# Kernel optimization log

Measured on AMD Instinct MI355X. Metric: run time of the kernel, lower is better.

The kernel has to match this reference:

```python
import jax, jax.numpy as jnp
import numpy as np
from jax import lax

L, C, H, W = 3, 64, 32, 32   # layer_num, new_size channels/spatial
N = H * W                    # 1024 attention positions
B = 8


def _conv(x, w, b, stride, pad):
    out = lax.conv_general_dilated(
        x, w, (stride, stride), [(pad, pad), (pad, pad)],
        dimension_numbers=('NCHW', 'OIHW', 'NCHW'))
    return out + b[None, :, None, None]


def setup_inputs() -> dict:
    key = jax.random.key(0)
    ks = iter(jax.random.split(key, 40))
    def rn(shape, scale=1.0):
        return (jax.random.normal(next(ks), shape) * scale).astype(jnp.float32)
    inp = {
        'src0': rn((B, 128, 64, 64)), 'src1': rn((B, 256, 32, 32)), 'src2': rn((B, 512, 32, 32)),
        'tgt0': rn((B, 128, 64, 64)), 'tgt1': rn((B, 256, 32, 32)), 'tgt2': rn((B, 512, 32, 32)),
    }
    # Project/Fit convs: layer0 is stride-2 3x3 (64->32), layers 1,2 are 1x1
    for pre, ic, k in [('fs0', 128, 3), ('fs1', 256, 1), ('fs2', 512, 1),
                       ('ft0', 128, 3), ('ft1', 256, 1), ('ft2', 512, 1)]:
        inp[pre + '_w'] = rn((C, ic, k, k), (ic * k * k) ** -0.5)
        inp[pre + '_b'] = rn((C,), 0.01)
    # PAM query/key/value and CAM value 1x1 convs, stacked over layers
    for pre in ['pq', 'pk', 'pv', 'cv']:
        inp[pre + '_w'] = rn((L, C, C), C ** -0.5)
        inp[pre + '_b'] = rn((L, C), 0.01)
    return inp


def reference(src0, src1, src2, tgt0, tgt1, tgt2,
              fs0_w, fs0_b, fs1_w, fs1_b, fs2_w, fs2_b,
              ft0_w, ft0_b, ft1_w, ft1_b, ft2_w, ft2_b,
              pq_w, pq_b, pk_w, pk_b, pv_w, pv_b, cv_w, cv_b):
    # Project: Fit each source/target to [B,C,H,W]
    S = jnp.stack([_conv(src0, fs0_w, fs0_b, 2, 1),
                   _conv(src1, fs1_w, fs1_b, 1, 0),
                   _conv(src2, fs2_w, fs2_b, 1, 0)])   # [L,B,C,H,W]
    T = jnp.stack([_conv(tgt0, ft0_w, ft0_b, 2, 1),
                   _conv(tgt1, ft1_w, ft1_b, 1, 0),
                   _conv(tgt2, ft2_w, ft2_b, 1, 0)])
    S = S.reshape(L, B, C, N)
    T = T.reshape(L, B, C, N)

    # ---- PAM: position attention over all (target i, source j) pairs ----
    q = jnp.einsum('ioc,ibcn->ibon', pq_w, T) + pq_b[:, None, :, None]
    k = jnp.einsum('joc,jbcn->jbon', pk_w, S) + pk_b[:, None, :, None]
    v = jnp.einsum('ioc,ibcn->ibon', pv_w, T) + pv_b[:, None, :, None]
    e_pam = jnp.einsum('ibcn,jbcm->ijbnm', q, k)          # [L,L,B,N,N]
    alpha_pam = jax.nn.softmax(lax.stop_gradient(e_pam.mean(axis=(2, 3, 4))), axis=-1)
    attn_pam = jax.nn.softmax(e_pam, axis=-1).sum(axis=1)  # sum over sources j -> [L,B,N,N]
    # out[b,c,n] = sum_m v[b,c,m] * attn[b,n,m]  (value @ attention^T)
    out_pam = jnp.einsum('ibcm,ibnm->ibcn', v, attn_pam)

    # ---- CAM: channel attention over all pairs ----
    e_cam = jnp.einsum('ibcn,jbdn->ijbcd', T, S)           # [L,L,B,C,C]
    alpha_cam = jax.nn.softmax(lax.stop_gradient(e_cam.mean(axis=(2, 3, 4))), axis=-1)
    attn_cam = jax.nn.softmax(e_cam, axis=-1).sum(axis=1)  # [L,B,C,C]
    vc = jnp.einsum('ioc,ibcn->ibon', cv_w, T) + cv_b[:, None, :, None]
    out_cam = jnp.einsum('ibcd,ibdn->ibcn', attn_cam, vc)

    fused = ((out_pam + out_cam) * 0.5).reshape(L, B, C * N)
    alpha = (alpha_cam + alpha_pam) * 0.5                  # [L,L]
    srcs = S.reshape(L, B, C * N)
    # DAAttention appends fused_i then projected target_i per layer (order preserved)
    tgts = jnp.stack([fused, T.reshape(L, B, C * N)], axis=1).reshape(2 * L, B, C * N)
    return (srcs, alpha, tgts)
```

## Files before the change

kernel.cpp:

```cpp
#include <hip/hip_runtime.h>

static constexpr int L_ = 3, B_ = 8, C_ = 64, N_ = 1024;
static constexpr int PLANE = C_ * N_;
static constexpr int SZ    = L_ * B_ * PLANE;
static constexpr int BPL   = B_ * PLANE;

#define DI __device__ __forceinline__

typedef _Float16 h8 __attribute__((ext_vector_type(8)));
typedef __attribute__((ext_vector_type(4))) float f32x4;
typedef unsigned int uint32;

DI float wred_sum(float v) {
#pragma unroll
  for (int m = 1; m < 64; m <<= 1) v += __shfl_xor(v, m, 64);
  return v;
}

DI unsigned short f2h(float f) {
  return __builtin_bit_cast(unsigned short, (_Float16)f);
}
DI float h2f(unsigned short h) {
  return (float)__builtin_bit_cast(_Float16, h);
}
DI uint32 pkh(float a, float b) {
  return (uint32)f2h(a) | ((uint32)f2h(b) << 16);
}
DI h8 bch8(uint4 v) { return __builtin_bit_cast(h8, v); }

DI f32x4 mfmah(h8 a, h8 b, f32x4 c) {
  return __builtin_amdgcn_mfma_f32_16x16x32_f16(a, b, c, 0, 0, 0);
}

DI void xprep_body(const float* __restrict__ ing, unsigned short* __restrict__ og,
                   int K, int N, int t, float tl[64][65])
{
#pragma unroll 4
  for (int r = 0; r < 16; ++r) {
    const int kk = r * 4 + (t >> 6);
    tl[kk][t & 63] = ing[(size_t)kk * N + (t & 63)];
  }
  __syncthreads();
  const int mm = t >> 2, kseg = (t & 3) * 16;
  uint32 hw[8];
#pragma unroll
  for (int ii = 0; ii < 8; ++ii)
    hw[ii] = pkh(tl[kseg + 2 * ii][mm], tl[kseg + 2 * ii + 1][mm]);
  unsigned short* o = og + (size_t)mm * K + kseg;
  uint4 h0; h0.x = hw[0]; h0.y = hw[1]; h0.z = hw[2]; h0.w = hw[3];
  uint4 h1; h1.x = hw[4]; h1.y = hw[5]; h1.z = hw[6]; h1.w = hw[7];
  *reinterpret_cast<uint4*>(o)     = h0;
  *reinterpret_cast<uint4*>(o + 8) = h1;
}

__global__ __launch_bounds__(256) void xprep_conv_kernel(
    const float* __restrict__ in_s, const float* __restrict__ in_t,
    unsigned short* __restrict__ o_s, unsigned short* __restrict__ o_t)
{
  __shared__ float tl[64][65];
  const int g = blockIdx.x & 7, ts = blockIdx.x >> 3;
  const int kc = blockIdx.y, nc = blockIdx.z;
  const float* in = ts ? in_t : in_s;
  unsigned short* out = ts ? o_t : o_s;
  const float* ing = in + (size_t)g * 128 * 4096 + (size_t)(kc * 64) * 4096 + nc * 64;
  unsigned short* og = out + ((size_t)g * 4096 + nc * 64) * 128 + kc * 64;
  xprep_body(ing, og, 128, 4096, threadIdx.x, tl);
}

__global__ __launch_bounds__(256) void xprep_fit_kernel(
    const float* __restrict__ s1, const float* __restrict__ s2,
    const float* __restrict__ t1, const float* __restrict__ t2,
    unsigned short* __restrict__ x1, unsigned short* __restrict__ x2,
    unsigned short* __restrict__ x3, unsigned short* __restrict__ x4)
{
  __shared__ float tl[64][65];
  const int g = blockIdx.x & 7, ts = blockIdx.x >> 3;
  const int K = (ts & 1) ? 512 : 256;
  const int kc = blockIdx.y, nc = blockIdx.z;
  if (kc >= (K >> 6)) return;
  const float* in = (ts == 0) ? s1 : (ts == 1) ? s2 : (ts == 2) ? t1 : t2;
  unsigned short* out = (ts == 0) ? x1 : (ts == 1) ? x2 : (ts == 2) ? x3 : x4;
  const float* ing = in + (size_t)g * K * 1024 + (size_t)(kc * 64) * 1024 + nc * 64;
  unsigned short* og = out + ((size_t)g * 1024 + nc * 64) * K + kc * 64;
  xprep_body(ing, og, K, 1024, threadIdx.x, tl);
}

__global__ __launch_bounds__(256) void w9conv_kernel(
    const float* __restrict__ w_s, const float* __restrict__ w_t,
    unsigned short* __restrict__ w9_s, unsigned short* __restrict__ w9_t)
{
  const int e = blockIdx.x * 256 + threadIdx.x;
  const float* w = (e < 73728) ? w_s : w_t;
  unsigned short* o = (e < 73728) ? w9_s : w9_t;
  const int le = (e < 73728) ? e : e - 73728;
  const int ci = le & 127;
  const int q = le >> 7;
  const int co = q & 63;
  const int k9 = q >> 6;
  o[le] = f2h(w[(co * 128 + ci) * 9 + k9]);
}

__global__ __launch_bounds__(256) void conv0_mfma_kernel(
    const unsigned short* __restrict__ inT_s, const unsigned short* __restrict__ inT_t,
    const unsigned short* __restrict__ w9_s, const unsigned short* __restrict__ w9_t,
    const float* __restrict__ b_s, const float* __restrict__ b_t,
    float* __restrict__ Sout, float* __restrict__ Tout, float* __restrict__ tdup)
{
  const int yr = blockIdx.x;
  const int b  = blockIdx.y;
  const int st = blockIdx.z;
  const unsigned short* inT = st ? inT_t : inT_s;
  const unsigned short* w9  = st ? w9_t  : w9_s;
  const float* bias = st ? b_t : b_s;
  float* outA = st ? Tout : Sout;

  const int t = threadIdx.x, lane = t & 63;
  const int ct = t >> 6;
  const int nl = lane & 15, g16 = lane >> 4;
  const unsigned short* inb = inT + (size_t)b * (4096 * 128);
  const unsigned short* wbase = w9 + (size_t)(ct * 16 + nl) * 128;

  f32x4 acc0 = f32x4{0.f, 0.f, 0.f, 0.f};
  f32x4 acc1 = f32x4{0.f, 0.f, 0.f, 0.f};
  const uint4 zz = uint4{0u, 0u, 0u, 0u};

#pragma unroll 1
  for (int tap = 0; tap < 9; ++tap) {
    const int ky = tap / 3, kx = tap - 3 * (tap / 3);
    const int py = 2 * yr - 1 + ky;
    const int px0 = 2 * nl - 1 + kx;
    const int px1 = px0 + 32;
    const bool v0 = (py >= 0) && (px0 >= 0);
    const bool v1 = (py >= 0);
    const unsigned short* prow = inb + (ptrdiff_t)py * (64 * 128);
#pragma unroll
    for (int ks = 0; ks < 4; ++ks) {
      const h8 a = bch8(*reinterpret_cast<const uint4*>(
          wbase + tap * 8192 + ks * 32 + g16 * 8));
      const uint4 bv0 = v0 ? *reinterpret_cast<const uint4*>(
                                 prow + px0 * 128 + ks * 32 + g16 * 8) : zz;
      const uint4 bv1 = v1 ? *reinterpret_cast<const uint4*>(
                                 prow + px1 * 128 + ks * 32 + g16 * 8) : zz;
      acc0 = mfmah(a, bch8(bv0), acc0);
      acc1 = mfmah(a, bch8(bv1), acc1);
    }
  }

  const int yb = yr * 32;
#pragma unroll
  for (int r = 0; r < 4; ++r) {
    const int co = ct * 16 + g16 * 4 + r;
    const float bv = bias[co];
    const int idx = (b * 64 + co) * 1024 + yb + nl;
    const float o0 = acc0[r] + bv;
    const float o1 = acc1[r] + bv;
    outA[idx] = o0; outA[idx + 16] = o1;
    if (st) { tdup[idx] = o0; tdup[idx + 16] = o1; }
  }
}

__global__ __launch_bounds__(256) void gemm64_kernel(
    const float* __restrict__ W, int wstride, int wdiv,
    const float* __restrict__ X, int xstride,
    float* __restrict__ out, int ostride,
    const float* __restrict__ bias, int bstride,
    int K)
{
  const int g  = blockIdx.x;
  const int n0 = blockIdx.y * 64;
  const float* Wg = W + (size_t)(g / wdiv) * wstride;
  const float* Xg = X + (size_t)g * xstride;
  const int t = threadIdx.x;
  __shared__ float Xs[32][64];
  __shared__ float Ws[32][64];
  const int tn = t & 15, cgp = t >> 4;
  const int n4 = tn * 4, co4 = cgp * 4;
  float acc[4][4] = {};

  for (int k0 = 0; k0 < K; k0 += 32) {
    {
      const int kk = t >> 4;
      const int nn = (t & 15) * 4;
      *reinterpret_cast<float4*>(&Xs[kk][nn]) =
          *reinterpret_cast<const float4*>(Xg + (size_t)(k0 + kk) * N_ + n0 + nn);
      *reinterpret_cast<float4*>(&Xs[kk + 16][nn]) =
          *reinterpret_cast<const float4*>(Xg + (size_t)(k0 + kk + 16) * N_ + n0 + nn);
    }
    {
      const int co = t & 63, q4 = t >> 6;
      const float* wp = Wg + (size_t)co * K + k0 + q4 * 8;
      const float4 a = *reinterpret_cast<const float4*>(wp);
      const float4 c = *reinterpret_cast<const float4*>(wp + 4);
      const int kb = q4 * 8;
      Ws[kb + 0][co] = a.x; Ws[kb + 1][co] = a.y; Ws[kb + 2][co] = a.z; Ws[kb + 3][co] = a.w;
      Ws[kb + 4][co] = c.x; Ws[kb + 5][co] = c.y; Ws[kb + 6][co] = c.z; Ws[kb + 7][co] = c.w;
    }
    __syncthreads();
#pragma unroll
    for (int kk = 0; kk < 32; ++kk) {
      const float4 xv = *reinterpret_cast<const float4*>(&Xs[kk][n4]);
      const float4 wv = *reinterpret_cast<const float4*>(&Ws[kk][co4]);
      const float xa[4] = {xv.x, xv.y, xv.z, xv.w};
      const float wa[4] = {wv.x, wv.y, wv.z, wv.w};
#pragma unroll
      for (int a = 0; a < 4; ++a)
#pragma unroll
        for (int b2 = 0; b2 < 4; ++b2)
          acc[a][b2] = fmaf(wa[a], xa[b2], acc[a][b2]);
    }
    __syncthreads();
  }

  float bv[4] = {0.f, 0.f, 0.f, 0.f};
  if (bias) {
    const float* bg = bias + (size_t)(g / wdiv) * bstride;
    bv[0] = bg[co4]; bv[1] = bg[co4 + 1]; bv[2] = bg[co4 + 2]; bv[3] = bg[co4 + 3];
  }
#pragma unroll
  for (int ii = 0; ii < 4; ++ii) {
    float4 o4;
    o4.x = acc[ii][0] + bv[ii]; o4.y = acc[ii][1] + bv[ii];
    o4.z = acc[ii][2] + bv[ii]; o4.w = acc[ii][3] + bv[ii];
    *reinterpret_cast<float4*>(out + (size_t)g * ostride + (co4 + ii) * N_ + n0 + n4) = o4;
  }
}

__global__ __launch_bounds__(256) void proj_kernel(
    const float* __restrict__ Tm, const float* __restrict__ Sm,
    const float* __restrict__ wq, const float* __restrict__ wk,
    const float* __restrict__ wv2, const float* __restrict__ wc,
    const float* __restrict__ bq, const float* __restrict__ bk,
    const float* __restrict__ bv2, const float* __restrict__ bc,
    unsigned short* __restrict__ qT, unsigned short* __restrict__ kT,
    unsigned short* __restrict__ vh, float* __restrict__ vcb)
{
  const int g  = blockIdx.x;
  const int n0 = blockIdx.y * 64;
  const int z  = blockIdx.z;
  const float* W  = (z == 0) ? wq : (z == 1) ? wk : (z == 2) ? wv2 : wc;
  const float* bi = (z == 0) ? bq : (z == 1) ? bk : (z == 2) ? bv2 : bc;
  const float* Xg = ((z == 1) ? Sm : Tm) + (size_t)g * PLANE;
  const float* Wg = W + (g >> 3) * 4096;
  const float* bg = bi + (g >> 3) * 64;

  const int t = threadIdx.x;
  __shared__ float Xs[32][64];
  __shared__ float Ws[32][64];
  const int tn = t & 15, cgp = t >> 4;
  const int n4 = tn * 4, co4 = cgp * 4;
  float acc[4][4] = {};

#pragma unroll 1
  for (int k0 = 0; k0 < 64; k0 += 32) {
    {
      const int kk = t >> 4;
      const int nn = (t & 15) * 4;
      *reinterpret_cast<float4*>(&Xs[kk][nn]) =
          *reinterpret_cast<const float4*>(Xg + (size_t)(k0 + kk) * N_ + n0 + nn);
      *reinterpret_cast<float4*>(&Xs[kk + 16][nn]) =
          *reinterpret_cast<const float4*>(Xg + (size_t)(k0 + kk + 16) * N_ + n0 + nn);
    }
    {
      const int co = t & 63, q4 = t >> 6;
      const float* wp = Wg + (size_t)co * 64 + k0 + q4 * 8;
      const float4 a = *reinterpret_cast<const float4*>(wp);
      const float4 c = *reinterpret_cast<const float4*>(wp + 4);
      const int kb = q4 * 8;
      Ws[kb + 0][co] = a.x; Ws[kb + 1][co] = a.y; Ws[kb + 2][co] = a.z; Ws[kb + 3][co] = a.w;
      Ws[kb + 4][co] = c.x; Ws[kb + 5][co] = c.y; Ws[kb + 6][co] = c.z; Ws[kb + 7][co] = c.w;
    }
    __syncthreads();
#pragma unroll
    for (int kk = 0; kk < 32; ++kk) {
      const float4 xv = *reinterpret_cast<const float4*>(&Xs[kk][n4]);
      const float4 wv = *reinterpret_cast<const float4*>(&Ws[kk][co4]);
      const float xa[4] = {xv.x, xv.y, xv.z, xv.w};
      const float wa[4] = {wv.x, wv.y, wv.z, wv.w};
#pragma unroll
      for (int a = 0; a < 4; ++a)
#pragma unroll
        for (int b2 = 0; b2 < 4; ++b2)
          acc[a][b2] = fmaf(wa[a], xa[b2], acc[a][b2]);
    }
    __syncthreads();
  }

  float bvv[4];
#pragma unroll
  for (int ii = 0; ii < 4; ++ii) bvv[ii] = bg[co4 + ii];

  if (z <= 1) {
    unsigned short* out = (z == 0 ? qT : kT);
#pragma unroll
    for (int jj = 0; jj < 4; ++jj) {
      const size_t base = ((size_t)g * 1024 + n0 + n4 + jj) * 64 + co4;
      uint2 w2;
      w2.x = pkh(acc[0][jj] + bvv[0], acc[1][jj] + bvv[1]);
      w2.y = pkh(acc[2][jj] + bvv[2], acc[3][jj] + bvv[3]);
      *reinterpret_cast<uint2*>(out + base) = w2;
    }
  } else if (z == 2) {
#pragma unroll
    for (int ii = 0; ii < 4; ++ii) {
      const size_t base = ((size_t)g * 64 + co4 + ii) * 1024 + n0 + n4;
      uint2 w2;
      w2.x = pkh(acc[ii][0] + bvv[ii], acc[ii][1] + bvv[ii]);
      w2.y = pkh(acc[ii][2] + bvv[ii], acc[ii][3] + bvv[ii]);
      *reinterpret_cast<uint2*>(vh + base) = w2;
    }
  } else {
    float* out = vcb + (size_t)g * PLANE;
#pragma unroll
    for (int ii = 0; ii < 4; ++ii) {
      float4 o4;
      o4.x = acc[ii][0] + bvv[ii]; o4.y = acc[ii][1] + bvv[ii];
      o4.z = acc[ii][2] + bvv[ii]; o4.w = acc[ii][3] + bvv[ii];
      *reinterpret_cast<float4*>(out + (co4 + ii) * N_ + n0 + n4) = o4;
    }
  }
}

__global__ __launch_bounds__(256) void whconv_kernel(
    const float* __restrict__ w1s, const float* __restrict__ w2s,
    const float* __restrict__ w1t, const float* __restrict__ w2t,
    unsigned short* __restrict__ wh)
{
  const int p = blockIdx.x * 256 + threadIdx.x;
  const float* in; int local; unsigned short* out;
  if (p < 8192)       { in = w1s; local = p;         out = wh; }
  else if (p < 24576) { in = w2s; local = p - 8192;  out = wh + 16384; }
  else if (p < 32768) { in = w1t; local = p - 24576; out = wh + 49152; }
  else                { in = w2t; local = p - 32768; out = wh + 65536; }
  const float2 v = *reinterpret_cast<const float2*>(in + 2 * local);
  *reinterpret_cast<uint32*>(out + 2 * local) = pkh(v.x, v.y);
}

__global__ __launch_bounds__(256) void gemmh_kernel(
    const unsigned short* __restrict__ Xa, const unsigned short* __restrict__ Xb,
    const unsigned short* __restrict__ Wa, const unsigned short* __restrict__ Wb,
    const float* __restrict__ ba, const float* __restrict__ bb,
    float* __restrict__ oa, float* __restrict__ ob, float* __restrict__ o2b,
    int K)
{
  const int g = blockIdx.x;
  const bool isb = g >= 8;
  const int gl = g & 7;
  const unsigned short* X = (isb ? Xb : Xa) + (size_t)gl * 1024 * K;
  const unsigned short* W = isb ? Wb : Wa;
  const float* bias = isb ? bb : ba;
  float* out = (isb ? ob : oa) + (size_t)gl * PLANE;
  float* out2 = isb ? o2b + (size_t)gl * PLANE : nullptr;

  const int t = threadIdx.x, lane = t & 63, wv = t >> 6;
  const int nl = lane & 15, g16 = lane >> 4;
  const int n0w = blockIdx.y * 64 + wv * 16;

  const unsigned short* xp = X + (size_t)(n0w + nl) * K + g16 * 8;
  const unsigned short* wp = W + (size_t)nl * K + g16 * 8;

  f32x4 acc[4];
#pragma unroll
  for (int ct = 0; ct < 4; ++ct) acc[ct] = f32x4{0.f, 0.f, 0.f, 0.f};

#pragma unroll 4
  for (int kk = 0; kk < K; kk += 32) {
    const h8 a = bch8(*reinterpret_cast<const uint4*>(xp + kk));
#pragma unroll
    for (int ct = 0; ct < 4; ++ct) {
      const h8 bfr = bch8(*reinterpret_cast<const uint4*>(wp + (size_t)ct * 16 * K + kk));
      acc[ct] = mfmah(a, bfr, acc[ct]);
    }
  }

#pragma unroll
  for (int ct = 0; ct < 4; ++ct) {
    const int co = ct * 16 + nl;
    const float bv = bias[co];
    float4 o4;
    o4.x = acc[ct][0] + bv; o4.y = acc[ct][1] + bv;
    o4.z = acc[ct][2] + bv; o4.w = acc[ct][3] + bv;
    const int idx = co * N_ + n0w + g16 * 4;
    *reinterpret_cast<float4*>(out + idx) = o4;
    if (out2) {
      out2[idx] = o4.x; out2[idx + 1] = o4.y;
      out2[idx + 2] = o4.z; out2[idx + 3] = o4.w;
    }
  }
}

__global__ __launch_bounds__(256) void ecam_kernel(
    const float* __restrict__ T, const float* __restrict__ S,
    float* __restrict__ ecam, float* __restrict__ esum_cam)
{
  const int bx = blockIdx.x;
  const int b = bx & 7;
  const int j = (bx >> 3) % 3;
  const int i = bx / 24;
  const int ych = blockIdx.y;
  const float* Tg = T + (size_t)(i * 8 + b) * PLANE;
  const float* Sg = S + (size_t)(j * 8 + b) * PLANE;
  const int t = threadIdx.x;
  __shared__ float Ts[64 * 68];
  __shared__ float Ss[64 * 68];
  __shared__ float rs[4];
  float acc[4][4] = {};
  const int c0 = (t & 15) * 4, d0 = (t >> 4) * 4;

  for (int nb = ych * 256; nb < ych * 256 + 256; nb += 64) {
    __syncthreads();
    {
      const int nn = t & 63, rb = t >> 6;
#pragma unroll
      for (int r = 0; r < 16; ++r) {
        const int row = rb * 16 + r;
        Ts[nn * 68 + row] = Tg[row * N_ + nb + nn];
        Ss[nn * 68 + row] = Sg[row * N_ + nb + nn];
      }
    }
    __syncthreads();
#pragma unroll 8
    for (int nn = 0; nn < 64; ++nn) {
      const float4 tv = *reinterpret_cast<const float4*>(&Ts[nn * 68 + c0]);
      const float4 sv = *reinterpret_cast<const float4*>(&Ss[nn * 68 + d0]);
      const float ta[4] = {tv.x, tv.y, tv.z, tv.w};
      const float sa[4] = {sv.x, sv.y, sv.z, sv.w};
#pragma unroll
      for (int ci = 0; ci < 4; ++ci)
#pragma unroll
        for (int di = 0; di < 4; ++di)
          acc[ci][di] = fmaf(ta[ci], sa[di], acc[ci][di]);
    }
  }
  float s = 0.f;
#pragma unroll
  for (int ci = 0; ci < 4; ++ci)
#pragma unroll
    for (int di = 0; di < 4; ++di) s += acc[ci][di];
  s = wred_sum(s);
  if ((t & 63) == 0) rs[t >> 6] = s;
  __syncthreads();
  if (t == 0) atomicAdd(esum_cam + i * 3 + j, rs[0] + rs[1] + rs[2] + rs[3]);

  float* eo = ecam + (size_t)((i * 3 + j) * 8 + b) * 4096;
#pragma unroll
  for (int ci = 0; ci < 4; ++ci)
#pragma unroll
    for (int di = 0; di < 4; ++di)
      atomicAdd(eo + (c0 + ci) * 64 + d0 + di, acc[ci][di]);
}

__global__ __launch_bounds__(256) void acam_kernel(
    const float* __restrict__ ecam, float* __restrict__ acam)
{
  const int bx = blockIdx.x;
  const int b = bx & 7, i = bx >> 3;
  const int t = threadIdx.x;
  const int c = t >> 2, seg = t & 3;
  float acc[16] = {};
#pragma unroll
  for (int j = 0; j < 3; ++j) {
    const float* e = ecam + (size_t)((i * 3 + j) * 8 + b) * 4096 + c * 64 + seg * 16;
    float ev[16];
#pragma unroll
    for (int r = 0; r < 4; ++r) {
      const float4 v4 = *reinterpret_cast<const float4*>(e + r * 4);
      ev[4 * r] = v4.x; ev[4 * r + 1] = v4.y; ev[4 * r + 2] = v4.z; ev[4 * r + 3] = v4.w;
    }
    float mx = ev[0];
#pragma unroll
    for (int r = 1; r < 16; ++r) mx = fmaxf(mx, ev[r]);
    mx = fmaxf(mx, __shfl_xor(mx, 1, 4));
    mx = fmaxf(mx, __shfl_xor(mx, 2, 4));
    float pv[16], ss = 0.f;
#pragma unroll
    for (int r = 0; r < 16; ++r) { pv[r] = __expf(ev[r] - mx); ss += pv[r]; }
    ss += __shfl_xor(ss, 1, 4);
    ss += __shfl_xor(ss, 2, 4);
    const float rc = 1.f / ss;
#pragma unroll
    for (int r = 0; r < 16; ++r) acc[r] += pv[r] * rc;
  }
  float* ao = acam + (size_t)(i * 8 + b) * 4096 + c * 64 + seg * 16;
#pragma unroll
  for (int r = 0; r < 4; ++r) {
    float4 o4; o4.x = acc[4 * r]; o4.y = acc[4 * r + 1]; o4.z = acc[4 * r + 2]; o4.w = acc[4 * r + 3];
    *reinterpret_cast<float4*>(ao + r * 4) = o4;
  }
}

__global__ __launch_bounds__(512, 4) void pam_mfma_kernel(
    const unsigned short* __restrict__ qT, const unsigned short* __restrict__ kT,
    const unsigned short* __restrict__ vh,
    const float* __restrict__ ocam, float* __restrict__ tgts, float* __restrict__ esum_pam)
{
  const int bx = blockIdx.x;
  const int qt = bx & 63;
  const int b  = (bx >> 6) & 7;
  const int i  = bx >> 9;
  const int n0 = qt * 16;
  const int t = threadIdx.x;
  const int lane = t & 63;
  const int wv = t >> 6;
  const int nl = lane & 15;
  const int g16 = lane >> 4;

  __shared__ unsigned short Plds[16 * 1024];
  __shared__ float osum[64 * 16];
  __shared__ float redmx[128];
  __shared__ float redse[128];
  __shared__ float redes[8];

  const size_t ibo = (size_t)(i * 8 + b) * PLANE;
  const size_t gbase = (size_t)(i * 8 + b) * 1024;

  const unsigned short* qp = qT + (gbase + n0 + nl) * 64 + g16 * 8;
  const h8 qh0 = bch8(*reinterpret_cast<const uint4*>(qp));
  const h8 qh1 = bch8(*reinterpret_cast<const uint4*>(qp + 32));

  const int wm0 = wv * 128;
  const int ct = wv & 3;
  const int mh = wv >> 2;

#pragma unroll 1
  for (int j = 0; j < 3; ++j) {
    const unsigned short* kp =
        kT + ((size_t)(j * 8 + b) * 1024 + wm0 + nl) * 64 + g16 * 8;

    f32x4 l4[8];
#pragma unroll
    for (int hh = 0; hh < 2; ++hh) {
      uint4 kf[8];
#pragma unroll
      for (int tt = 0; tt < 4; ++tt) {
        const int off = (hh * 4 + tt) * 1024;
        kf[2 * tt]     = *reinterpret_cast<const uint4*>(kp + off);
        kf[2 * tt + 1] = *reinterpret_cast<const uint4*>(kp + off + 32);
      }
#pragma unroll
      for (int tt = 0; tt < 4; ++tt) {
        f32x4 a = f32x4{0.f, 0.f, 0.f, 0.f};
        a = mfmah(bch8(kf[2 * tt]), qh0, a);
        a = mfmah(bch8(kf[2 * tt + 1]), qh1, a);
        l4[hh * 4 + tt] = a;
      }
    }

    float pm = -3.4e38f, es = 0.f;
#pragma unroll
    for (int tt = 0; tt < 8; ++tt) {
#pragma unroll
      for (int r = 0; r < 4; ++r) { pm = fmaxf(pm, l4[tt][r]); es += l4[tt][r]; }
    }
    pm = fmaxf(pm, __shfl_xor(pm, 16, 64));
    pm = fmaxf(pm, __shfl_xor(pm, 32, 64));
    es = wred_sum(es);
    if (lane < 16) redmx[wv * 16 + lane] = pm;
    if (lane == 0) redes[wv] = es;
    __syncthreads();
    float mx = redmx[nl];
#pragma unroll
    for (int w = 1; w < 8; ++w) mx = fmaxf(mx, redmx[w * 16 + nl]);
    if (t == 0) {
      float s = 0.f;
#pragma unroll
      for (int w = 0; w < 8; ++w) s += redes[w];
      atomicAdd(esum_pam + i * 3 + j, s);
    }

    float ps = 0.f;
#pragma unroll
    for (int tt = 0; tt < 8; ++tt) {
#pragma unroll
      for (int r = 0; r < 4; ++r) {
        l4[tt][r] = __expf(l4[tt][r] - mx);
        ps += l4[tt][r];
      }
    }
    ps += __shfl_xor(ps, 16, 64);
    ps += __shfl_xor(ps, 32, 64);
    if (lane < 16) redse[wv * 16 + lane] = ps;
    __syncthreads();
    float den = redse[nl];
#pragma unroll
    for (int w = 1; w < 8; ++w) den += redse[w * 16 + nl];
    const float rs = 1.f / den;

#pragma unroll
    for (int tt = 0; tt < 8; ++tt) {
      const int m = wm0 + tt * 16 + g16 * 4;
      unsigned short* pp = &Plds[nl * 1024 + (m ^ (nl * 8))];
      float p0 = l4[tt][0] * rs, p1 = l4[tt][1] * rs;
      float p2 = l4[tt][2] * rs, p3 = l4[tt][3] * rs;
      if (j > 0) {
        const uint2 old = *reinterpret_cast<const uint2*>(pp);
        p0 += h2f((unsigned short)(old.x & 0xffffu));
        p1 += h2f((unsigned short)(old.x >> 16));
        p2 += h2f((unsigned short)(old.y & 0xffffu));
        p3 += h2f((unsigned short)(old.y >> 16));
      }
      uint2 w2; w2.x = pkh(p0, p1); w2.y = pkh(p2, p3);
      *reinterpret_cast<uint2*>(pp) = w2;
    }
  }

  __syncthreads();

  const unsigned short* vg = vh + ibo + (size_t)(ct * 16 + nl) * 1024 + mh * 512 + g16 * 8;
  f32x4 oa = f32x4{0.f, 0.f, 0.f, 0.f};
#pragma unroll
  for (int hh = 0; hh < 2; ++hh) {
    uint4 vf[8];
#pragma unroll
    for (int u = 0; u < 8; ++u)
      vf[u] = *reinterpret_cast<const uint4*>(vg + (hh * 8 + u) * 32);
#pragma unroll
    for (int u = 0; u < 8; ++u) {
      const int ml = mh * 512 + (hh * 8 + u) * 32 + g16 * 8;
      const uint4 pf = *reinterpret_cast<const uint4*>(&Plds[nl * 1024 + (ml ^ (nl * 8))]);
      oa = mfmah(bch8(vf[u]), bch8(pf), oa);
    }
  }

  if (mh == 0) {
#pragma unroll
    for (int r = 0; r < 4; ++r)
      osum[(ct * 16 + g16 * 4 + r) * 16 + nl] = oa[r];
  }
  __syncthreads();
  if (mh == 1) {
    const float* og = ocam + ibo;
    float* outg = tgts + (size_t)(2 * i * 8 + b) * PLANE;
#pragma unroll
    for (int r = 0; r < 4; ++r) {
      const int c = ct * 16 + g16 * 4 + r;
      const int idx = c * N_ + n0 + nl;
      outg[idx] = 0.5f * (oa[r] + osum[c * 16 + nl] + og[idx]);
    }
  }
}

__global__ void alpha_kernel(const float* __restrict__ esum, float* __restrict__ alpha)
{
  const int t = threadIdx.x;
  if (t >= 9) return;
  const int i = t / 3, j = t % 3;
  float p[3], c[3];
#pragma unroll
  for (int jj = 0; jj < 3; ++jj) {
    p[jj] = esum[i * 3 + jj] * (1.0f / 8388608.0f);
    c[jj] = esum[9 + i * 3 + jj] * (1.0f / 32768.0f);
  }
  const float mp = fmaxf(p[0], fmaxf(p[1], p[2]));
  const float mc = fmaxf(c[0], fmaxf(c[1], c[2]));
  float sp = 0.f, sc = 0.f;
#pragma unroll
  for (int jj = 0; jj < 3; ++jj) { sp += __expf(p[jj] - mp); sc += __expf(c[jj] - mc); }
  alpha[t] = 0.5f * (__expf(p[j] - mp) / sp + __expf(c[j] - mc) / sc);
}

extern "C" void kernel_launch(void* const* d_in, const int* in_sizes, int n_in,
                              void* d_out, int out_size, void* d_ws, size_t ws_size,
                              hipStream_t stream)
{
  const float* src0 = (const float*)d_in[0];
  const float* src1 = (const float*)d_in[1];
  const float* src2 = (const float*)d_in[2];
  const float* tgt0 = (const float*)d_in[3];
  const float* tgt1 = (const float*)d_in[4];
  const float* tgt2 = (const float*)d_in[5];
  const float* fs0_w = (const float*)d_in[6];  const float* fs0_b = (const float*)d_in[7];
  const float* fs1_w = (const float*)d_in[8];  const float* fs1_b = (const float*)d_in[9];
  const float* fs2_w = (const float*)d_in[10]; const float* fs2_b = (const float*)d_in[11];
  const float* ft0_w = (const float*)d_in[12]; const float* ft0_b = (const float*)d_in[13];
  const float* ft1_w = (const float*)d_in[14]; const float* ft1_b = (const float*)d_in[15];
  const float* ft2_w = (const float*)d_in[16]; const float* ft2_b = (const float*)d_in[17];
  const float* pq_w = (const float*)d_in[18];  const float* pq_b = (const float*)d_in[19];
  const float* pk_w = (const float*)d_in[20];  const float* pk_b = (const float*)d_in[21];
  const float* pv_w = (const float*)d_in[22];  const float* pv_b = (const float*)d_in[23];
  const float* cv_w = (const float*)d_in[24];  const float* cv_b = (const float*)d_in[25];

  float* out = (float*)d_out;
  float* S     = out;
  float* alpha = out + SZ;
  float* tgts  = out + SZ + 9;

  float* ws   = (float*)d_ws;
  float* T    = ws;
  float* qb   = ws + (size_t)SZ;
  float* kb   = ws + (size_t)2 * SZ;
  float* vcb  = ws + (size_t)4 * SZ;
  float* ocam = ws + (size_t)5 * SZ;
  float* ecam = ws + (size_t)6 * SZ;
  float* acam = ws + (size_t)6 * SZ + 294912;
  float* esum = ws + (size_t)6 * SZ + 393216;

  unsigned short* kT = (unsigned short*)(ws + (size_t)6 * SZ + 393216 + 256);
  unsigned short* vh = kT + (size_t)24 * PLANE;
  unsigned short* wh = vh + (size_t)24 * PLANE;
  unsigned short* w9s = wh + 98304;
  unsigned short* w9t = w9s + 73728;
  unsigned short* qT = (unsigned short*)kb;

  unsigned short* inTs = (unsigned short*)qb;
  unsigned short* inTt = inTs + 4194304;
  unsigned short* Xs1 = (unsigned short*)qb;
  unsigned short* Xs2 = Xs1 + 2097152;
  unsigned short* Xt1 = Xs1 + 6291456;
  unsigned short* Xt2 = Xs1 + 8388608;

  hipMemsetAsync(esum, 0, 18 * sizeof(float), stream);
  hipMemsetAsync(ecam, 0, 294912 * sizeof(float), stream);

  w9conv_kernel<<<576, 256, 0, stream>>>(fs0_w, ft0_w, w9s, w9t);
  xprep_conv_kernel<<<dim3(16, 2, 64), 256, 0, stream>>>(src0, tgt0, inTs, inTt);
  conv0_mfma_kernel<<<dim3(32, 8, 2), 256, 0, stream>>>(
      inTs, inTt, w9s, w9t, fs0_b, ft0_b, S, T, tgts + (size_t)1 * BPL);

  xprep_fit_kernel<<<dim3(32, 8, 16), 256, 0, stream>>>(
      src1, src2, tgt1, tgt2, Xs1, Xs2, Xt1, Xt2);
  whconv_kernel<<<192, 256, 0, stream>>>(fs1_w, fs2_w, ft1_w, ft2_w, wh);
  gemmh_kernel<<<dim3(16, 16), 256, 0, stream>>>(
      Xs1, Xt1, wh, wh + 49152, fs1_b, ft1_b,
      S + BPL, T + BPL, tgts + (size_t)3 * BPL, 256);
  gemmh_kernel<<<dim3(16, 16), 256, 0, stream>>>(
      Xs2, Xt2, wh + 16384, wh + 65536, fs2_b, ft2_b,
      S + 2 * BPL, T + 2 * BPL, tgts + (size_t)5 * BPL, 512);

  proj_kernel<<<dim3(24, 16, 4), 256, 0, stream>>>(
      T, S, pq_w, pk_w, pv_w, cv_w, pq_b, pk_b, pv_b, cv_b, qT, kT, vh, vcb);

  ecam_kernel<<<dim3(72, 4), 256, 0, stream>>>(T, S, ecam, esum + 9);
  acam_kernel<<<24, 256, 0, stream>>>(ecam, acam);
  gemm64_kernel<<<dim3(24, 16), 256, 0, stream>>>(acam, 4096, 1, vcb, PLANE, ocam, PLANE,
                                                  nullptr, 0, 64);

  pam_mfma_kernel<<<1536, 512, 0, stream>>>(qT, kT, vh, ocam, tgts, esum);

  alpha_kernel<<<1, 64, 0, stream>>>(esum, alpha);
}
```

Baseline: 296.8 us.

## Merge weight-prep and 1x1 GEMM launches; single-barrier online softmax in PAM

The two weight-conversion kernels become one launch, and the two gemmh launches for the K=256 and K=512 fit convs become a single grid that picks its operands from the block index. This cuts kernel launches and lets the two GEMMs share the GPU. In the PAM kernel, each wave now computes exp against its own local max and its own partial sum before the barrier. The block-wide max and denominator are then combined with a rescale, which removes one __syncthreads per source layer. The reduction arrays are double-buffered so the next iteration cannot overwrite values still being read, at the cost of some extra exp work per thread.

After: 292.1 us. Within noise of the previous version (-1.6%).

```diff
diff --git a/kernel.cpp b/kernel.cpp
--- a/kernel.cpp
+++ b/kernel.cpp
@@ -85,19 +85,33 @@
   xprep_body(ing, og, K, 1024, threadIdx.x, tl);
 }
 
-__global__ __launch_bounds__(256) void w9conv_kernel(
+__global__ __launch_bounds__(256) void wprep_kernel(
     const float* __restrict__ w_s, const float* __restrict__ w_t,
-    unsigned short* __restrict__ w9_s, unsigned short* __restrict__ w9_t)
+    unsigned short* __restrict__ w9_s, unsigned short* __restrict__ w9_t,
+    const float* __restrict__ w1s, const float* __restrict__ w2s,
+    const float* __restrict__ w1t, const float* __restrict__ w2t,
+    unsigned short* __restrict__ wh)
 {
   const int e = blockIdx.x * 256 + threadIdx.x;
-  const float* w = (e < 73728) ? w_s : w_t;
-  unsigned short* o = (e < 73728) ? w9_s : w9_t;
-  const int le = (e < 73728) ? e : e - 73728;
-  const int ci = le & 127;
-  const int q = le >> 7;
-  const int co = q & 63;
-  const int k9 = q >> 6;
-  o[le] = f2h(w[(co * 128 + ci) * 9 + k9]);
+  if (e < 147456) {
+    const float* w = (e < 73728) ? w_s : w_t;
+    unsigned short* o = (e < 73728) ? w9_s : w9_t;
+    const int le = (e < 73728) ? e : e - 73728;
+    const int ci = le & 127;
+    const int q = le >> 7;
+    const int co = q & 63;
+    const int k9 = q >> 6;
+    o[le] = f2h(w[(co * 128 + ci) * 9 + k9]);
+  } else {
+    const int p = e - 147456;
+    const float* in; int local; unsigned short* out;
+    if (p < 8192)       { in = w1s; local = p;         out = wh; }
+    else if (p < 24576) { in = w2s; local = p - 8192;  out = wh + 16384; }
+    else if (p < 32768) { in = w1t; local = p - 24576; out = wh + 49152; }
+    else                { in = w2t; local = p - 32768; out = wh + 65536; }
+    const float2 v = *reinterpret_cast<const float2*>(in + 2 * local);
+    *reinterpret_cast<uint32*>(out + 2 * local) = pkh(v.x, v.y);
+  }
 }
 
 __global__ __launch_bounds__(256) void conv0_mfma_kernel(
@@ -320,36 +334,28 @@
   }
 }
 
-__global__ __launch_bounds__(256) void whconv_kernel(
-    const float* __restrict__ w1s, const float* __restrict__ w2s,
-    const float* __restrict__ w1t, const float* __restrict__ w2t,
-    unsigned short* __restrict__ wh)
-{
-  const int p = blockIdx.x * 256 + threadIdx.x;
-  const float* in; int local; unsigned short* out;
-  if (p < 8192)       { in = w1s; local = p;         out = wh; }
-  else if (p < 24576) { in = w2s; local = p - 8192;  out = wh + 16384; }
-  else if (p < 32768) { in = w1t; local = p - 24576; out = wh + 49152; }
-  else                { in = w2t; local = p - 32768; out = wh + 65536; }
-  const float2 v = *reinterpret_cast<const float2*>(in + 2 * local);
-  *reinterpret_cast<uint32*>(out + 2 * local) = pkh(v.x, v.y);
-}
-
 __global__ __launch_bounds__(256) void gemmh_kernel(
-    const unsigned short* __restrict__ Xa, const unsigned short* __restrict__ Xb,
-    const unsigned short* __restrict__ Wa, const unsigned short* __restrict__ Wb,
-    const float* __restrict__ ba, const float* __restrict__ bb,
-    float* __restrict__ oa, float* __restrict__ ob, float* __restrict__ o2b,
-    int K)
-{
-  const int g = blockIdx.x;
+    const unsigned short* __restrict__ X1s, const unsigned short* __restrict__ X1t,
+    const unsigned short* __restrict__ X2s, const unsigned short* __restrict__ X2t,
+    const unsigned short* __restrict__ wh,
+    const float* __restrict__ b1s, const float* __restrict__ b1t,
+    const float* __restrict__ b2s, const float* __restrict__ b2t,
+    float* __restrict__ S, float* __restrict__ T,
+    float* __restrict__ tdup3, float* __restrict__ tdup5)
+{
+  const int gx = blockIdx.x;
+  const bool k5 = gx >= 16;
+  const int g = gx & 15;
   const bool isb = g >= 8;
   const int gl = g & 7;
-  const unsigned short* X = (isb ? Xb : Xa) + (size_t)gl * 1024 * K;
-  const unsigned short* W = isb ? Wb : Wa;
-  const float* bias = isb ? bb : ba;
-  float* out = (isb ? ob : oa) + (size_t)gl * PLANE;
-  float* out2 = isb ? o2b + (size_t)gl * PLANE : nullptr;
+  const int K = k5 ? 512 : 256;
+  const unsigned short* X = (k5 ? (isb ? X2t : X2s) : (isb ? X1t : X1s))
+                            + (size_t)gl * 1024 * K;
+  const unsigned short* W = wh + (k5 ? (isb ? 65536 : 16384) : (isb ? 49152 : 0));
+  const float* bias = k5 ? (isb ? b2t : b2s) : (isb ? b1t : b1s);
+  float* out = (k5 ? (isb ? T + 2 * BPL : S + 2 * BPL) : (isb ? T + BPL : S + BPL))
+               + (size_t)gl * PLANE;
+  float* out2 = isb ? (k5 ? tdup5 : tdup3) + (size_t)gl * PLANE : nullptr;
 
   const int t = threadIdx.x, lane = t & 63, wv = t >> 6;
   const int nl = lane & 15, g16 = lane >> 4;
@@ -506,9 +512,9 @@
 
   __shared__ unsigned short Plds[16 * 1024];
   __shared__ float osum[64 * 16];
-  __shared__ float redmx[128];
-  __shared__ float redse[128];
-  __shared__ float redes[8];
+  __shared__ float redmx[2][128];
+  __shared__ float redse[2][128];
+  __shared__ float redes[2][8];
 
   const size_t ibo = (size_t)(i * 8 + b) * PLANE;
   const size_t gbase = (size_t)(i * 8 + b) * 1024;
@@ -523,6 +529,7 @@
 
 #pragma unroll 1
   for (int j = 0; j < 3; ++j) {
+    const int pj = j & 1;
     const unsigned short* kp =
         kT + ((size_t)(j * 8 + b) * 1024 + wm0 + nl) * 64 + g16 * 8;
 
@@ -554,43 +561,45 @@
     pm = fmaxf(pm, __shfl_xor(pm, 16, 64));
     pm = fmaxf(pm, __shfl_xor(pm, 32, 64));
     es = wred_sum(es);
-    if (lane < 16) redmx[wv * 16 + lane] = pm;
-    if (lane == 0) redes[wv] = es;
+
+    float ps = 0.f;
+#pragma unroll
+    for (int tt = 0; tt < 8; ++tt) {
+#pragma unroll
+      for (int r = 0; r < 4; ++r) {
+        l4[tt][r] = __expf(l4[tt][r] - pm);
+        ps += l4[tt][r];
+      }
+    }
+    ps += __shfl_xor(ps, 16, 64);
+    ps += __shfl_xor(ps, 32, 64);
+
+    if (lane < 16) { redmx[pj][wv * 16 + lane] = pm; redse[pj][wv * 16 + lane] = ps; }
+    if (lane == 0) redes[pj][wv] = es;
     __syncthreads();
-    float mx = redmx[nl];
-#pragma unroll
-    for (int w = 1; w < 8; ++w) mx = fmaxf(mx, redmx[w * 16 + nl]);
+
+    float mx = redmx[pj][nl];
+#pragma unroll
+    for (int w = 1; w < 8; ++w) mx = fmaxf(mx, redmx[pj][w * 16 + nl]);
+    float den = 0.f;
+#pragma unroll
+    for (int w = 0; w < 8; ++w)
+      den += redse[pj][w * 16 + nl] * __expf(redmx[pj][w * 16 + nl] - mx);
+    const float sc = __expf(pm - mx) / den;
+
     if (t == 0) {
       float s = 0.f;
 #pragma unroll
-      for (int w = 0; w < 8; ++w) s += redes[w];
+      for (int w = 0; w < 8; ++w) s += redes[pj][w];
       atomicAdd(esum_pam + i * 3 + j, s);
     }
-
-    float ps = 0.f;
-#pragma unroll
-    for (int tt = 0; tt < 8; ++tt) {
-#pragma unroll
-      for (int r = 0; r < 4; ++r) {
-        l4[tt][r] = __expf(l4[tt][r] - mx);
-        ps += l4[tt][r];
-      }
-    }
-    ps += __shfl_xor(ps, 16, 64);
-    ps += __shfl_xor(ps, 32, 64);
-    if (lane < 16) redse[wv * 16 + lane] = ps;
-    __syncthreads();
-    float den = redse[nl];
-#pragma unroll
-    for (int w = 1; w < 8; ++w) den += redse[w * 16 + nl];
-    const float rs = 1.f / den;
 
 #pragma unroll
     for (int tt = 0; tt < 8; ++tt) {
       const int m = wm0 + tt * 16 + g16 * 4;
       unsigned short* pp = &Plds[nl * 1024 + (m ^ (nl * 8))];
-      float p0 = l4[tt][0] * rs, p1 = l4[tt][1] * rs;
-      float p2 = l4[tt][2] * rs, p3 = l4[tt][3] * rs;
+      float p0 = l4[tt][0] * sc, p1 = l4[tt][1] * sc;
+      float p2 = l4[tt][2] * sc, p3 = l4[tt][3] * sc;
       if (j > 0) {
         const uint2 old = *reinterpret_cast<const uint2*>(pp);
         p0 += h2f((unsigned short)(old.x & 0xffffu));
@@ -711,20 +720,18 @@
   hipMemsetAsync(esum, 0, 18 * sizeof(float), stream);
   hipMemsetAsync(ecam, 0, 294912 * sizeof(float), stream);
 
-  w9conv_kernel<<<576, 256, 0, stream>>>(fs0_w, ft0_w, w9s, w9t);
+  wprep_kernel<<<768, 256, 0, stream>>>(fs0_w, ft0_w, w9s, w9t,
+                                        fs1_w, fs2_w, ft1_w, ft2_w, wh);
+
   xprep_conv_kernel<<<dim3(16, 2, 64), 256, 0, stream>>>(src0, tgt0, inTs, inTt);
   conv0_mfma_kernel<<<dim3(32, 8, 2), 256, 0, stream>>>(
       inTs, inTt, w9s, w9t, fs0_b, ft0_b, S, T, tgts + (size_t)1 * BPL);
 
   xprep_fit_kernel<<<dim3(32, 8, 16), 256, 0, stream>>>(
       src1, src2, tgt1, tgt2, Xs1, Xs2, Xt1, Xt2);
-  whconv_kernel<<<192, 256, 0, stream>>>(fs1_w, fs2_w, ft1_w, ft2_w, wh);
-  gemmh_kernel<<<dim3(16, 16), 256, 0, stream>>>(
-      Xs1, Xt1, wh, wh + 49152, fs1_b, ft1_b,
-      S + BPL, T + BPL, tgts + (size_t)3 * BPL, 256);
-  gemmh_kernel<<<dim3(16, 16), 256, 0, stream>>>(
-      Xs2, Xt2, wh + 16384, wh + 65536, fs2_b, ft2_b,
-      S + 2 * BPL, T + 2 * BPL, tgts + (size_t)5 * BPL, 512);
+  gemmh_kernel<<<dim3(32, 16), 256, 0, stream>>>(
+      Xs1, Xt1, Xs2, Xt2, wh, fs1_b, ft1_b, fs2_b, ft2_b,
+      S, T, tgts + (size_t)3 * BPL, tgts + (size_t)5 * BPL);
 
   proj_kernel<<<dim3(24, 16, 4), 256, 0, stream>>>(
       T, S, pq_w, pk_w, pv_w, cv_w, pq_b, pk_b, pv_b, cv_b, qT, kT, vh, vcb);
```
